# Kernel optimization log

Hardware: AMD Instinct MI355X
Metric: run time of the kernel (lower is better)

The kernel has to match this reference:

```python
import jax, jax.numpy as jnp
import numpy as np

B, K, H = 512, 160, 256
ALPHA = 0.5          # fgw_alpha
TEMP = 2.0           # consistency temperature
MAX_SPAN = 30        # max_span_len
L_FGW, L_SPAN, L_CONS = 0.1, 0.5, 0.3


def setup_inputs() -> dict:
    key = jax.random.key(0)
    ks = jax.random.split(key, 12)
    gamma = jax.random.uniform(ks[0], (B, K, K), jnp.float32) / K  # transport-plan scale
    return {
        "en_node_emb": jax.random.normal(ks[1], (B, K, H), jnp.float32),
        "vi_node_emb": jax.random.normal(ks[2], (B, K, H), jnp.float32),
        "gamma": gamma,
        "D_en": jax.random.uniform(ks[3], (B, K, K), jnp.float32),
        "D_vi": jax.random.uniform(ks[4], (B, K, K), jnp.float32),
        "M": jax.random.uniform(ks[5], (B, K, K), jnp.float32),
        "en_start": jax.random.randint(ks[6], (B,), 0, K, jnp.int64 if jax.config.read('jax_enable_x64') else jnp.int32),
        "en_end": jax.random.randint(ks[7], (B,), 0, K, jnp.int64 if jax.config.read('jax_enable_x64') else jnp.int32),
        "w_start": jax.random.normal(ks[8], (H, 1), jnp.float32) * 0.02,
        "b_start": jnp.zeros((1,), jnp.float32),
        "w_end": jax.random.normal(ks[9], (H, 1), jnp.float32) * 0.02,
        "b_end": jnp.zeros((1,), jnp.float32),
    }


def _qa_head(emb, w_s, b_s, w_e, b_e):
    # emb: (B,K,H) -> logits (B,K)
    start = (emb @ w_s).squeeze(-1) + b_s
    end = (emb @ w_e).squeeze(-1) + b_e
    return start, end


def _ce(logits, labels):
    # mean cross-entropy, labels always valid after clamping
    logp = jax.nn.log_softmax(logits, axis=-1)
    return -jnp.take_along_axis(logp, labels[:, None], axis=-1).squeeze(-1)


def _fgw_loss(gamma, D_en, D_vi, M, alpha):
    w = jnp.sum(M * gamma, axis=(1, 2))
    p = gamma.sum(axis=2)  # (B,K)
    q = gamma.sum(axis=1)  # (B,K)
    gw1 = jnp.einsum('bij,bi,bj->b', D_en ** 2, p, p)
    gw2 = jnp.einsum('bij,bi,bj->b', D_vi ** 2, q, q)
    t = jnp.einsum('bik,bkl->bil', D_en, gamma)       # C1 @ g
    t = jnp.einsum('bil,bjl->bij', t, D_vi)           # (C1 @ g) @ C2^T
    gw3 = jnp.sum(t * gamma, axis=(1, 2))
    return jnp.mean(alpha * (gw1 + gw2 - 2.0 * gw3) + (1.0 - alpha) * w)


def _decode_span(gamma, en_start, en_end, k, max_span):
    # pseudo-label decode (no-grad in original) -> (B,) int start/end
    idx = jnp.arange(k)
    s = jnp.clip(en_start, 0, k - 1)
    e = jnp.maximum(s, jnp.clip(en_end, 0, k - 1))
    row_mask = (idx[None, :] >= s[:, None]) & (idx[None, :] <= e[:, None])  # (B,K)
    vi_score = jnp.einsum('bi,bij->bj', row_mask.astype(gamma.dtype), gamma)  # (B,K)
    pair = vi_score[:, :, None] + vi_score[:, None, :]  # (B, si, ei)
    span = idx[None, :] - idx[:, None]                  # ei - si
    valid = (span >= 0) & (span <= max_span)
    pair = jnp.where(valid[None], pair, -jnp.inf)
    flat = jnp.argmax(pair.reshape(pair.shape[0], -1), axis=-1)
    best_s, best_e = flat // k, flat % k
    unanswerable = (en_start == 0) & (en_end == 0)
    best_s = jnp.where(unanswerable, 0, best_s)
    best_e = jnp.where(unanswerable, 0, best_e)
    return best_s, best_e


def _kl_batchmean(vi_logp, en_logp):
    # KL(target=exp(en_logp) || vi) with torch kl_div(batchmean) semantics
    p = jnp.exp(en_logp)
    return jnp.sum(p * (en_logp - vi_logp)) / p.shape[0]


def reference(en_node_emb, vi_node_emb, gamma, D_en, D_vi, M, en_start, en_end,
              w_start, b_start, w_end, b_end):
    en_sl, en_el = _qa_head(en_node_emb, w_start, b_start, w_end, b_end)
    vi_sl, vi_el = _qa_head(vi_node_emb, w_start, b_start, w_end, b_end)

    # QA loss (EN supervised, positions clamped into [0, K-1])
    s_lab = jnp.clip(en_start, 0, K - 1)
    e_lab = jnp.clip(en_end, 0, K - 1)
    l_qa = (jnp.mean(_ce(en_sl, s_lab)) + jnp.mean(_ce(en_el, e_lab))) / 2.0

    # FGW alignment
    l_fgw = _fgw_loss(gamma, D_en, D_vi, M, ALPHA)

    # Span projection (pseudo labels via stop-gradient on gamma)
    ps, pe = _decode_span(jax.lax.stop_gradient(gamma), en_start, en_end, K, MAX_SPAN)
    answerable = ((en_start > 0) | (en_end > 0)).astype(jnp.float32)
    n_ans = jnp.sum(answerable)
    ce_span = (_ce(vi_sl, ps) + _ce(vi_el, pe)) / 2.0  # (B,)
    l_span = jnp.where(n_ans > 0, jnp.sum(ce_span * answerable) / jnp.maximum(n_ans, 1.0), 0.0)

    # Consistency (EN detached)
    en_s_log = jax.nn.log_softmax(jax.lax.stop_gradient(en_sl) / TEMP, axis=-1)
    en_e_log = jax.nn.log_softmax(jax.lax.stop_gradient(en_el) / TEMP, axis=-1)
    vi_s_log = jax.nn.log_softmax(vi_sl / TEMP, axis=-1)
    vi_e_log = jax.nn.log_softmax(vi_el / TEMP, axis=-1)
    l_cons = TEMP ** 2 * (_kl_batchmean(vi_s_log, en_s_log) + _kl_batchmean(vi_e_log, en_e_log)) / 2.0

    total = l_qa + L_FGW * l_fgw + L_SPAN * l_span + L_CONS * l_cons
    return total, l_qa, l_fgw, l_span, l_cons
```

## Files before the change

### kernel.cpp

```cpp
#include <hip/hip_runtime.h>

#define Bn 512
#define Kn 160
#define Hn 256
#define ALPHA 0.5f
#define MAX_SPAN 30
#define L_FGW 0.1f
#define L_SPAN 0.5f
#define L_CONS 0.3f
#define KP 16
#define NP 10

typedef __bf16 bf16x8 __attribute__((ext_vector_type(8)));
typedef float f32x16 __attribute__((ext_vector_type(16)));
typedef float f32x4v __attribute__((ext_vector_type(4)));

struct PhS {
  float prow[160][41];
  float qcol[25][160];
  float vcol[25][160];
  float psh[160], qsh[160], vscsh[160];
  float esh[160], eeh[160], vssh[160], veh[160];
  float wsh[16], g1sh[16], g2sh[16];
  float bv[256];
  int bidx[256];
  int pspe[2];
};
struct FgS {
  __bf16 sDen[2][2][Kn][8];
  __bf16 sG[2][2][Kn][8];
  __bf16 sGT[2][2][Kn][8];
  __bf16 sVT[2][2][Kn][8];
  float red[16];
};

__device__ __forceinline__ void wg_barrier() {
  asm volatile("s_waitcnt lgkmcnt(0)" ::: "memory");
  __builtin_amdgcn_s_barrier();
  __builtin_amdgcn_sched_barrier(0);
}

__global__ __launch_bounds__(1024, 4) void mega_k(
    const float* __restrict__ en, const float* __restrict__ vi,
    const float* __restrict__ w_s, const float* __restrict__ b_s,
    const float* __restrict__ w_e, const float* __restrict__ b_e,
    const float* __restrict__ gam, const float* __restrict__ M,
    const float* __restrict__ Den, const float* __restrict__ Dvi,
    const int* __restrict__ enst, const int* __restrict__ enen,
    float* __restrict__ sp1) {
  __shared__ __align__(16) char shraw[sizeof(PhS)];
  PhS& S = *(PhS*)shraw;
  FgS& F = *(FgS*)shraw;
  int b = blockIdx.x;
  int tid = threadIdx.x;
  int wv = tid >> 6, lane = tid & 63;
  const float* gam_b = gam + (size_t)b * 25600;
  const float* m_b   = M   + (size_t)b * 25600;
  const float* den_b = Den + (size_t)b * 25600;
  const float* dvi_b = Dvi + (size_t)b * 25600;
  int s0 = enst[b], e0 = enen[b];
  int s = min(max(s0, 0), Kn - 1);
  int e = max(s, min(max(e0, 0), Kn - 1));
  bool act = tid < 1000;
  int c = tid % 40, rg = tid / 40;

  float q4[4] = {0.f,0.f,0.f,0.f}, v4[4] = {0.f,0.f,0.f,0.f};
  float wloc = 0.f;
  #pragma unroll
  for (int i = 0; i < 7; ++i) {
    int r = rg + 25 * i;
    if (act && r < 160) {
      float4 g = *(const float4*)(gam_b + (size_t)r * 160 + 4 * c);
      f32x4v m = __builtin_nontemporal_load((const f32x4v*)(m_b + (size_t)r * 160 + 4 * c));
      wloc += m[0]*g.x + m[1]*g.y + m[2]*g.z + m[3]*g.w;
      S.prow[r][c] = g.x + g.y + g.z + g.w;
      q4[0]+=g.x; q4[1]+=g.y; q4[2]+=g.z; q4[3]+=g.w;
      float f = (r >= s && r <= e) ? 1.f : 0.f;
      v4[0]+=f*g.x; v4[1]+=f*g.y; v4[2]+=f*g.z; v4[3]+=f*g.w;
    }
  }
  if (act) {
    #pragma unroll
    for (int j = 0; j < 4; ++j) { S.qcol[rg][4*c+j] = q4[j]; S.vcol[rg][4*c+j] = v4[j]; }
  }
  #pragma unroll
  for (int o = 32; o; o >>= 1) wloc += __shfl_xor(wloc, o);
  if (lane == 0) S.wsh[wv] = wloc;
  __syncthreads();
  if (tid < 160) {
    float sp = 0.f;
    #pragma unroll 8
    for (int c2 = 0; c2 < 40; ++c2) sp += S.prow[tid][c2];
    S.psh[tid] = sp;
    float sq = 0.f, sv = 0.f;
    #pragma unroll 5
    for (int k = 0; k < 25; ++k) { sq += S.qcol[k][tid]; sv += S.vcol[k][tid]; }
    S.qsh[tid] = sq;
    S.vscsh[tid] = sv;
  }
  __syncthreads();

  float g1loc = 0.f, g2loc = 0.f;
  {
    float pc0=0,pc1=0,pc2=0,pc3=0,qc0=0,qc1=0,qc2=0,qc3=0;
    if (act) {
      pc0=S.psh[4*c]; pc1=S.psh[4*c+1]; pc2=S.psh[4*c+2]; pc3=S.psh[4*c+3];
      qc0=S.qsh[4*c]; qc1=S.qsh[4*c+1]; qc2=S.qsh[4*c+2]; qc3=S.qsh[4*c+3];
    }
    #pragma unroll
    for (int i = 0; i < 7; ++i) {
      int r = rg + 25 * i;
      if (act && r < 160) {
        float4 d = *(const float4*)(den_b + (size_t)r * 160 + 4 * c);
        g1loc += S.psh[r] * (d.x*d.x*pc0 + d.y*d.y*pc1 + d.z*d.z*pc2 + d.w*d.w*pc3);
        float4 v = *(const float4*)(dvi_b + (size_t)r * 160 + 4 * c);
        g2loc += S.qsh[r] * (v.x*v.x*qc0 + v.y*v.y*qc1 + v.z*v.z*qc2 + v.w*v.w*qc3);
      }
    }
  }
  #pragma unroll
  for (int o = 32; o; o >>= 1) { g1loc += __shfl_xor(g1loc, o); g2loc += __shfl_xor(g2loc, o); }
  if (lane == 0) { S.g1sh[wv] = g1loc; S.g2sh[wv] = g2loc; }

  {
    float4 ws4 = *(const float4*)(w_s + lane * 4);
    float4 we4 = *(const float4*)(w_e + lane * 4);
    float bs0 = b_s[0], be0 = b_e[0];
    const float* en_b = en + (size_t)b * 40960;
    const float* vi_b = vi + (size_t)b * 40960;
    #pragma unroll
    for (int rr = 0; rr < 10; ++rr) {
      int row = wv * 10 + rr;
      f32x4v ev = __builtin_nontemporal_load((const f32x4v*)(en_b + (size_t)row * 256 + lane * 4));
      f32x4v vv = __builtin_nontemporal_load((const f32x4v*)(vi_b + (size_t)row * 256 + lane * 4));
      float a0 = ev[0]*ws4.x + ev[1]*ws4.y + ev[2]*ws4.z + ev[3]*ws4.w;
      float a1 = ev[0]*we4.x + ev[1]*we4.y + ev[2]*we4.z + ev[3]*we4.w;
      float a2 = vv[0]*ws4.x + vv[1]*ws4.y + vv[2]*ws4.z + vv[3]*ws4.w;
      float a3 = vv[0]*we4.x + vv[1]*we4.y + vv[2]*we4.z + vv[3]*we4.w;
      #pragma unroll
      for (int o = 32; o; o >>= 1) {
        a0 += __shfl_xor(a0, o); a1 += __shfl_xor(a1, o);
        a2 += __shfl_xor(a2, o); a3 += __shfl_xor(a3, o);
      }
      if (lane == 0) {
        S.esh[row] = a0 + bs0;  S.eeh[row] = a1 + be0;
        S.vssh[row] = a2 + bs0; S.veh[row] = a3 + be0;
      }
    }
  }
  __syncthreads();

  float best = -1e30f;
  int bfl = 0x7fffffff;
  if (tid < 160) {
    float vsi = S.vscsh[tid];
    int hi = min(tid + MAX_SPAN, Kn - 1);
    for (int ei = tid; ei <= hi; ++ei) {
      float v = vsi + S.vscsh[ei];
      if (v > best) { best = v; bfl = tid * Kn + ei; }
    }
  }
  if (tid < 256) { S.bv[tid] = best; S.bidx[tid] = bfl; }
  for (int st = 128; st > 0; st >>= 1) {
    __syncthreads();
    if (tid < st) {
      float v2 = S.bv[tid + st]; int i2 = S.bidx[tid + st];
      if (v2 > S.bv[tid] || (v2 == S.bv[tid] && i2 < S.bidx[tid])) { S.bv[tid] = v2; S.bidx[tid] = i2; }
    }
  }
  if (tid == 0) {
    int fl = S.bidx[0];
    int ps = fl / Kn, pe = fl - (fl / Kn) * Kn;
    if (s0 == 0 && e0 == 0) { ps = 0; pe = 0; }
    S.pspe[0] = ps; S.pspe[1] = pe;
    float sw = 0.f, s1 = 0.f, s2 = 0.f;
    #pragma unroll
    for (int i = 0; i < 16; ++i) { sw += S.wsh[i]; s1 += S.g1sh[i]; s2 += S.g2sh[i]; }
    float* o = sp1 + (size_t)b * 12;
    o[4] = sw; o[7] = s1; o[8] = s2;
  }
  __syncthreads();
  if (wv == 0) {
    float xes[3], xee[3], xvs[3], xve[3];
    #pragma unroll
    for (int j = 0; j < 3; ++j) {
      int idx = lane + 64 * j;
      bool val = idx < Kn;
      xes[j] = val ? S.esh[idx] : -1e30f;
      xee[j] = val ? S.eeh[idx] : -1e30f;
      xvs[j] = val ? S.vssh[idx] : -1e30f;
      xve[j] = val ? S.veh[idx] : -1e30f;
    }
    auto wlse = [&](float x0, float x1, float x2) -> float {
      float m = fmaxf(fmaxf(x0, x1), x2);
      #pragma unroll
      for (int o = 32; o; o >>= 1) m = fmaxf(m, __shfl_xor(m, o));
      float su = expf(x0 - m) + expf(x1 - m) + expf(x2 - m);
      #pragma unroll
      for (int o = 32; o; o >>= 1) su += __shfl_xor(su, o);
      return m + logf(su);
    };
    float l_es = wlse(xes[0], xes[1], xes[2]);
    float l_ee = wlse(xee[0], xee[1], xee[2]);
    float l_vs = wlse(xvs[0], xvs[1], xvs[2]);
    float l_ve = wlse(xve[0], xve[1], xve[2]);
    float lT_es = wlse(xes[0]*0.5f, xes[1]*0.5f, xes[2]*0.5f);
    float lT_ee = wlse(xee[0]*0.5f, xee[1]*0.5f, xee[2]*0.5f);
    float lT_vs = wlse(xvs[0]*0.5f, xvs[1]*0.5f, xvs[2]*0.5f);
    float lT_ve = wlse(xve[0]*0.5f, xve[1]*0.5f, xve[2]*0.5f);
    float kls = 0.f, kle = 0.f;
    #pragma unroll
    for (int j = 0; j < 3; ++j) {
      int idx = lane + 64 * j;
      if (idx < Kn) {
        float aa = xes[j]*0.5f - lT_es;
        float bb = xvs[j]*0.5f - lT_vs;
        kls += expf(aa) * (aa - bb);
        float cc = xee[j]*0.5f - lT_ee;
        float dd = xve[j]*0.5f - lT_ve;
        kle += expf(cc) * (cc - dd);
      }
    }
    #pragma unroll
    for (int o = 32; o; o >>= 1) { kls += __shfl_xor(kls, o); kle += __shfl_xor(kle, o); }
    if (lane == 0) {
      int sl = min(max(s0, 0), Kn - 1);
      int el = min(max(e0, 0), Kn - 1);
      float* o = sp1 + (size_t)b * 12;
      o[0] = l_es - S.esh[sl];
      o[1] = l_ee - S.eeh[el];
      o[2] = kls;
      o[3] = kle;
      bool answerable = (s0 > 0) || (e0 > 0);
      float ce = 0.5f * ((l_vs - S.vssh[S.pspe[0]]) + (l_ve - S.veh[S.pspe[1]]));
      o[5] = answerable ? ce : 0.f;
      o[6] = answerable ? 1.f : 0.f;
    }
  }
  __syncthreads();

  bool rm0 = tid < 640;
  const float* s0p;
  __bf16 *d00, *d01;
  if (rm0) {
    int op = tid >= 320 ? 1 : 0;
    int fr = tid - 320 * op;
    int cc = fr >= 160 ? 1 : 0;
    int r = fr - 160 * cc;
    s0p = (op ? gam_b : den_b) + (size_t)r * 160 + 8 * cc;
    d00 = op ? &F.sG[0][cc][r][0] : &F.sDen[0][cc][r][0];
    d01 = op ? &F.sG[1][cc][r][0] : &F.sDen[1][cc][r][0];
  } else {
    int f3 = tid - 640;
    int op = f3 >= 320 ? 1 : 0;
    int f4 = f3 - 320 * op;
    int cc = f4 >= 160 ? 1 : 0;
    int j = f4 - 160 * cc;
    s0p = (op ? dvi_b : gam_b) + (size_t)(8 * cc) * 160 + j;
    d00 = op ? &F.sVT[0][cc][j][0] : &F.sGT[0][cc][j][0];
    d01 = op ? &F.sVT[1][cc][j][0] : &F.sGT[1][cc][j][0];
  }
  bool act1 = tid < 256;
  int f5 = tid + 64;
  int cc1 = f5 >= 160 ? 1 : 0;
  int j1 = f5 - 160 * cc1;
  const float* s1p = dvi_b + (size_t)(8 * cc1) * 160 + j1;
  __bf16* d10 = &F.sVT[0][cc1][j1][0];
  __bf16* d11 = &F.sVT[1][cc1][j1][0];

  float vA0[8], vA1[8], vB0[8], vB1[8];
  auto load0 = [&](int p, float* v) {
    if (rm0) {
      const float* sp = s0p + p * KP;
      float4 x = *(const float4*)sp;
      float4 y = *(const float4*)(sp + 4);
      v[0]=x.x; v[1]=x.y; v[2]=x.z; v[3]=x.w;
      v[4]=y.x; v[5]=y.y; v[6]=y.z; v[7]=y.w;
    } else {
      const float* sp = s0p + (size_t)p * KP * 160;
      #pragma unroll
      for (int e2 = 0; e2 < 8; ++e2) v[e2] = sp[(size_t)e2 * 160];
    }
  };
  auto load1 = [&](int p, float* v) {
    if (!act1) return;
    const float* sp = s1p + (size_t)p * KP * 160;
    #pragma unroll
    for (int e2 = 0; e2 < 8; ++e2) v[e2] = sp[(size_t)e2 * 160];
  };
  auto wr = [&](const float* v0, const float* v1, __bf16* w0, __bf16* w1) {
    bf16x8 wv2;
    #pragma unroll
    for (int e2 = 0; e2 < 8; ++e2) wv2[e2] = (__bf16)v0[e2];
    *(bf16x8*)w0 = wv2;
    if (act1) {
      bf16x8 wv3;
      #pragma unroll
      for (int e2 = 0; e2 < 8; ++e2) wv3[e2] = (__bf16)v1[e2];
      *(bf16x8*)w1 = wv3;
    }
  };

  int ra = lane & 31, cc2 = lane >> 5;
  int t0 = wv;
  int ti0 = t0 / 5, tj0 = t0 - 5 * (t0 / 5);
  int rowa0 = ti0 * 32 + ra, rowb0 = tj0 * 32 + ra;
  int t1 = wv + 16;
  bool val1t = t1 < 25;
  int ti1 = t1 / 5, tj1 = t1 - 5 * (t1 / 5);
  int rowa1 = ti1 * 32 + ra, rowb1 = tj1 * 32 + ra;
  f32x16 acc10 = {}, acc20 = {}, acc11 = {}, acc21 = {};
  auto mf = [&](int BUF) {
    {
      bf16x8 a1 = *(const bf16x8*)&F.sDen[BUF][cc2][rowa0][0];
      bf16x8 b1 = *(const bf16x8*)&F.sGT[BUF][cc2][rowb0][0];
      bf16x8 a2 = *(const bf16x8*)&F.sG[BUF][cc2][rowa0][0];
      bf16x8 b2 = *(const bf16x8*)&F.sVT[BUF][cc2][rowb0][0];
      acc10 = __builtin_amdgcn_mfma_f32_32x32x16_bf16(a1, b1, acc10, 0, 0, 0);
      acc20 = __builtin_amdgcn_mfma_f32_32x32x16_bf16(a2, b2, acc20, 0, 0, 0);
    }
    if (val1t) {
      bf16x8 a1 = *(const bf16x8*)&F.sDen[BUF][cc2][rowa1][0];
      bf16x8 b1 = *(const bf16x8*)&F.sGT[BUF][cc2][rowb1][0];
      bf16x8 a2 = *(const bf16x8*)&F.sG[BUF][cc2][rowa1][0];
      bf16x8 b2 = *(const bf16x8*)&F.sVT[BUF][cc2][rowb1][0];
      acc11 = __builtin_amdgcn_mfma_f32_32x32x16_bf16(a1, b1, acc11, 0, 0, 0);
      acc21 = __builtin_amdgcn_mfma_f32_32x32x16_bf16(a2, b2, acc21, 0, 0, 0);
    }
  };

  load0(0, vA0); load1(0, vA1);
  load0(1, vB0); load1(1, vB1);
  wr(vA0, vA1, d00, d10);
  __syncthreads();
  for (int p = 0; p < NP; p += 2) {
    if (p + 2 < NP) { load0(p + 2, vA0); load1(p + 2, vA1); }
    mf(0);
    wr(vB0, vB1, d01, d11);
    wg_barrier();
    if (p + 3 < NP) { load0(p + 3, vB0); load1(p + 3, vB1); }
    mf(1);
    if (p + 2 < NP) wr(vA0, vA1, d00, d10);
    wg_barrier();
  }
  float g3 = 0.f;
  #pragma unroll
  for (int r2 = 0; r2 < 16; ++r2) g3 += acc10[r2] * acc20[r2];
  if (val1t) {
    #pragma unroll
    for (int r2 = 0; r2 < 16; ++r2) g3 += acc11[r2] * acc21[r2];
  }
  #pragma unroll
  for (int o = 32; o; o >>= 1) g3 += __shfl_xor(g3, o);
  if (lane == 0) F.red[wv] = g3;
  __syncthreads();
  if (tid == 0) {
    float s3 = 0.f;
    #pragma unroll
    for (int i = 0; i < 16; ++i) s3 += F.red[i];
    sp1[(size_t)b * 12 + 9] = s3;
  }
}

__global__ __launch_bounds__(512) void finalize_k(
    const float* __restrict__ sp1, float* __restrict__ out) {
  __shared__ float red[8][10];
  int tid = threadIdx.x;
  int wid = tid >> 6, lane = tid & 63;
  float v[10];
  const float* a = sp1 + (size_t)tid * 12;
  #pragma unroll
  for (int i = 0; i < 10; ++i) v[i] = a[i];
  #pragma unroll
  for (int i = 0; i < 10; ++i) {
    float s = v[i];
    #pragma unroll
    for (int o = 32; o; o >>= 1) s += __shfl_xor(s, o);
    v[i] = s;
  }
  if (lane == 0) {
    #pragma unroll
    for (int i = 0; i < 10; ++i) red[wid][i] = v[i];
  }
  __syncthreads();
  if (tid == 0) {
    float t[10];
    #pragma unroll
    for (int i = 0; i < 10; ++i) {
      float s = 0.f;
      #pragma unroll
      for (int w2 = 0; w2 < 8; ++w2) s += red[w2][i];
      t[i] = s;
    }
    float ce_s = t[0], ce_e = t[1], kls = t[2], kle = t[3];
    float w = t[4], spn = t[5], nans = t[6];
    float gw1 = t[7], gw2 = t[8], gw3 = t[9];
    float l_qa = (ce_s + ce_e) / (2.f * Bn);
    float l_fgw = (ALPHA * (gw1 + gw2 - 2.f * gw3) + (1.f - ALPHA) * w) / Bn;
    float l_span = (nans > 0.f) ? spn / fmaxf(nans, 1.f) : 0.f;
    float l_cons = 2.f * (kls + kle) / Bn;
    float total = l_qa + L_FGW * l_fgw + L_SPAN * l_span + L_CONS * l_cons;
    out[0] = total; out[1] = l_qa; out[2] = l_fgw; out[3] = l_span; out[4] = l_cons;
  }
}

extern "C" void kernel_launch(void* const* d_in, const int* in_sizes, int n_in,
                              void* d_out, int out_size, void* d_ws, size_t ws_size,
                              hipStream_t stream) {
  const float* en  = (const float*)d_in[0];
  const float* vi  = (const float*)d_in[1];
  const float* gam = (const float*)d_in[2];
  const float* Den = (const float*)d_in[3];
  const float* Dvi = (const float*)d_in[4];
  const float* M   = (const float*)d_in[5];
  const int* enst  = (const int*)d_in[6];
  const int* enen  = (const int*)d_in[7];
  const float* w_s = (const float*)d_in[8];
  const float* b_s = (const float*)d_in[9];
  const float* w_e = (const float*)d_in[10];
  const float* b_e = (const float*)d_in[11];
  float* sp1 = (float*)d_ws;
  float* out = (float*)d_out;

  mega_k<<<Bn, 1024, 0, stream>>>(en, vi, w_s, b_s, w_e, b_e, gam, M, Den, Dvi,
                                  enst, enen, sp1);
  finalize_k<<<1, 512, 0, stream>>>(sp1, out);
}
```

Measured before the change: 118.2 us.

## Interleave QA-head embedding loads with gamma pass and remap rows to 640 threads

Moves the en/vi embedding dot-product loop into the first gamma/M pass, so the embedding loads are in flight alongside the gamma and M loads instead of running after the D pass. Remaps the gamma, M, D_en and D_vi row work from 1000 active threads over 25 row groups (7 iterations, with tail guards) to 640 threads over 16 row groups (10 iterations, no tail guards), which also shrinks the qcol/vcol shared buffers. This raises memory-level parallelism early in the kernel. In exchange, fewer threads take part in the streaming loads and register pressure in the fused loop goes up.

Result: faster. 109.8 us (-7.1%).

```diff
diff --git a/kernel.cpp b/kernel.cpp
--- a/kernel.cpp
+++ b/kernel.cpp
@@ -17,8 +17,8 @@
 
 struct PhS {
   float prow[160][41];
-  float qcol[25][160];
-  float vcol[25][160];
+  float qcol[16][160];
+  float vcol[16][160];
   float psh[160], qsh[160], vscsh[160];
   float esh[160], eeh[160], vssh[160], veh[160];
   float wsh[16], g1sh[16], g2sh[16];
@@ -61,15 +61,23 @@
   int s0 = enst[b], e0 = enen[b];
   int s = min(max(s0, 0), Kn - 1);
   int e = max(s, min(max(e0, 0), Kn - 1));
-  bool act = tid < 1000;
-  int c = tid % 40, rg = tid / 40;
-
+  bool actA = tid < 640;
+  int rm = tid / 40, c = tid - 40 * rm;
+
+  float4 ws4 = *(const float4*)(w_s + lane * 4);
+  float4 we4 = *(const float4*)(w_e + lane * 4);
+  float bs0 = b_s[0], be0 = b_e[0];
+  const float* en_b = en + (size_t)b * 40960;
+  const float* vi_b = vi + (size_t)b * 40960;
   float q4[4] = {0.f,0.f,0.f,0.f}, v4[4] = {0.f,0.f,0.f,0.f};
   float wloc = 0.f;
   #pragma unroll
-  for (int i = 0; i < 7; ++i) {
-    int r = rg + 25 * i;
-    if (act && r < 160) {
+  for (int it = 0; it < 10; ++it) {
+    int crow = wv * 10 + it;
+    f32x4v ev = __builtin_nontemporal_load((const f32x4v*)(en_b + (size_t)crow * 256 + lane * 4));
+    f32x4v vv = __builtin_nontemporal_load((const f32x4v*)(vi_b + (size_t)crow * 256 + lane * 4));
+    if (actA) {
+      int r = 16 * it + rm;
       float4 g = *(const float4*)(gam_b + (size_t)r * 160 + 4 * c);
       f32x4v m = __builtin_nontemporal_load((const f32x4v*)(m_b + (size_t)r * 160 + 4 * c));
       wloc += m[0]*g.x + m[1]*g.y + m[2]*g.z + m[3]*g.w;
@@ -78,10 +86,23 @@
       float f = (r >= s && r <= e) ? 1.f : 0.f;
       v4[0]+=f*g.x; v4[1]+=f*g.y; v4[2]+=f*g.z; v4[3]+=f*g.w;
     }
-  }
-  if (act) {
-    #pragma unroll
-    for (int j = 0; j < 4; ++j) { S.qcol[rg][4*c+j] = q4[j]; S.vcol[rg][4*c+j] = v4[j]; }
+    float a0 = ev[0]*ws4.x + ev[1]*ws4.y + ev[2]*ws4.z + ev[3]*ws4.w;
+    float a1 = ev[0]*we4.x + ev[1]*we4.y + ev[2]*we4.z + ev[3]*we4.w;
+    float a2 = vv[0]*ws4.x + vv[1]*ws4.y + vv[2]*ws4.z + vv[3]*ws4.w;
+    float a3 = vv[0]*we4.x + vv[1]*we4.y + vv[2]*we4.z + vv[3]*we4.w;
+    #pragma unroll
+    for (int o = 32; o; o >>= 1) {
+      a0 += __shfl_xor(a0, o); a1 += __shfl_xor(a1, o);
+      a2 += __shfl_xor(a2, o); a3 += __shfl_xor(a3, o);
+    }
+    if (lane == 0) {
+      S.esh[crow] = a0 + bs0;  S.eeh[crow] = a1 + be0;
+      S.vssh[crow] = a2 + bs0; S.veh[crow] = a3 + be0;
+    }
+  }
+  if (actA) {
+    #pragma unroll
+    for (int j = 0; j < 4; ++j) { S.qcol[rm][4*c+j] = q4[j]; S.vcol[rm][4*c+j] = v4[j]; }
   }
   #pragma unroll
   for (int o = 32; o; o >>= 1) wloc += __shfl_xor(wloc, o);
@@ -93,61 +114,29 @@
     for (int c2 = 0; c2 < 40; ++c2) sp += S.prow[tid][c2];
     S.psh[tid] = sp;
     float sq = 0.f, sv = 0.f;
-    #pragma unroll 5
-    for (int k = 0; k < 25; ++k) { sq += S.qcol[k][tid]; sv += S.vcol[k][tid]; }
+    #pragma unroll 4
+    for (int k = 0; k < 16; ++k) { sq += S.qcol[k][tid]; sv += S.vcol[k][tid]; }
     S.qsh[tid] = sq;
     S.vscsh[tid] = sv;
   }
   __syncthreads();
 
   float g1loc = 0.f, g2loc = 0.f;
-  {
-    float pc0=0,pc1=0,pc2=0,pc3=0,qc0=0,qc1=0,qc2=0,qc3=0;
-    if (act) {
-      pc0=S.psh[4*c]; pc1=S.psh[4*c+1]; pc2=S.psh[4*c+2]; pc3=S.psh[4*c+3];
-      qc0=S.qsh[4*c]; qc1=S.qsh[4*c+1]; qc2=S.qsh[4*c+2]; qc3=S.qsh[4*c+3];
-    }
-    #pragma unroll
-    for (int i = 0; i < 7; ++i) {
-      int r = rg + 25 * i;
-      if (act && r < 160) {
-        float4 d = *(const float4*)(den_b + (size_t)r * 160 + 4 * c);
-        g1loc += S.psh[r] * (d.x*d.x*pc0 + d.y*d.y*pc1 + d.z*d.z*pc2 + d.w*d.w*pc3);
-        float4 v = *(const float4*)(dvi_b + (size_t)r * 160 + 4 * c);
-        g2loc += S.qsh[r] * (v.x*v.x*qc0 + v.y*v.y*qc1 + v.z*v.z*qc2 + v.w*v.w*qc3);
-      }
+  if (actA) {
+    float pc0=S.psh[4*c], pc1=S.psh[4*c+1], pc2=S.psh[4*c+2], pc3=S.psh[4*c+3];
+    float qc0=S.qsh[4*c], qc1=S.qsh[4*c+1], qc2=S.qsh[4*c+2], qc3=S.qsh[4*c+3];
+    #pragma unroll
+    for (int k = 0; k < 10; ++k) {
+      int r = 16 * k + rm;
+      float4 d = *(const float4*)(den_b + (size_t)r * 160 + 4 * c);
+      g1loc += S.psh[r] * (d.x*d.x*pc0 + d.y*d.y*pc1 + d.z*d.z*pc2 + d.w*d.w*pc3);
+      float4 v = *(const float4*)(dvi_b + (size_t)r * 160 + 4 * c);
+      g2loc += S.qsh[r] * (v.x*v.x*qc0 + v.y*v.y*qc1 + v.z*v.z*qc2 + v.w*v.w*qc3);
     }
   }
   #pragma unroll
   for (int o = 32; o; o >>= 1) { g1loc += __shfl_xor(g1loc, o); g2loc += __shfl_xor(g2loc, o); }
   if (lane == 0) { S.g1sh[wv] = g1loc; S.g2sh[wv] = g2loc; }
-
-  {
-    float4 ws4 = *(const float4*)(w_s + lane * 4);
-    float4 we4 = *(const float4*)(w_e + lane * 4);
-    float bs0 = b_s[0], be0 = b_e[0];
-    const float* en_b = en + (size_t)b * 40960;
-    const float* vi_b = vi + (size_t)b * 40960;
-    #pragma unroll
-    for (int rr = 0; rr < 10; ++rr) {
-      int row = wv * 10 + rr;
-      f32x4v ev = __builtin_nontemporal_load((const f32x4v*)(en_b + (size_t)row * 256 + lane * 4));
-      f32x4v vv = __builtin_nontemporal_load((const f32x4v*)(vi_b + (size_t)row * 256 + lane * 4));
-      float a0 = ev[0]*ws4.x + ev[1]*ws4.y + ev[2]*ws4.z + ev[3]*ws4.w;
-      float a1 = ev[0]*we4.x + ev[1]*we4.y + ev[2]*we4.z + ev[3]*we4.w;
-      float a2 = vv[0]*ws4.x + vv[1]*ws4.y + vv[2]*ws4.z + vv[3]*ws4.w;
-      float a3 = vv[0]*we4.x + vv[1]*we4.y + vv[2]*we4.z + vv[3]*we4.w;
-      #pragma unroll
-      for (int o = 32; o; o >>= 1) {
-        a0 += __shfl_xor(a0, o); a1 += __shfl_xor(a1, o);
-        a2 += __shfl_xor(a2, o); a3 += __shfl_xor(a3, o);
-      }
-      if (lane == 0) {
-        S.esh[row] = a0 + bs0;  S.eeh[row] = a1 + be0;
-        S.vssh[row] = a2 + bs0; S.veh[row] = a3 + be0;
-      }
-    }
-  }
   __syncthreads();
 
   float best = -1e30f;
```
